# Optimization experiments

Measured on AMD Instinct MI355X. Metric: run time of the kernel, lower is better.

## Reference

```python
import jax, jax.numpy as jnp
import numpy as np

D = 64          # embed_dim
NH = 4          # nhead
DH = D // NH    # head dim
FF = 2048       # TransformerEncoderLayer default dim_feedforward
V = 1_000_000   # vocab (num items)
MAX_LEN = 50
INSERT_LEN = 10
EPS = 1e-5
N_LAYERS = 2


def setup_inputs() -> dict:
    key = jax.random.key(0)
    ks = jax.random.split(key, 8)
    s = 0.02
    return {
        "ht": jax.random.normal(ks[0], (D,), dtype=jnp.float32),
        "item_emb": jax.random.normal(ks[1], (V, D), dtype=jnp.float32) * s,
        "pos_emb": jax.random.normal(ks[2], (MAX_LEN, D), dtype=jnp.float32) * s,
        "in_proj_w": jax.random.normal(ks[3], (N_LAYERS, 3 * D, D), dtype=jnp.float32) * s,
        "in_proj_b": jnp.zeros((N_LAYERS, 3 * D), jnp.float32),
        "out_w": jax.random.normal(ks[4], (N_LAYERS, D, D), dtype=jnp.float32) * s,
        "out_b": jnp.zeros((N_LAYERS, D), jnp.float32),
        "ln1_w": jnp.ones((N_LAYERS, D), jnp.float32),
        "ln1_b": jnp.zeros((N_LAYERS, D), jnp.float32),
        "ln2_w": jnp.ones((N_LAYERS, D), jnp.float32),
        "ln2_b": jnp.zeros((N_LAYERS, D), jnp.float32),
        "ffn1_w": jax.random.normal(ks[5], (N_LAYERS, FF, D), dtype=jnp.float32) * s,
        "ffn1_b": jnp.zeros((N_LAYERS, FF), jnp.float32),
        "ffn2_w": jax.random.normal(ks[6], (N_LAYERS, D, FF), dtype=jnp.float32) * s,
        "ffn2_b": jnp.zeros((N_LAYERS, D), jnp.float32),
    }


def _ln(x, w, b):
    m = jnp.mean(x, axis=-1, keepdims=True)
    v = jnp.mean(jnp.square(x - m), axis=-1, keepdims=True)
    return (x - m) * jax.lax.rsqrt(v + EPS) * w + b


def _encoder_layer(x, ipw, ipb, ow, ob, l1w, l1b, l2w, l2b, f1w, f1b, f2w, f2b):
    # x: [S, D]; post-norm TransformerEncoderLayer (PyTorch defaults, eval mode)
    S = x.shape[0]
    qkv = x @ ipw.T + ipb                      # [S, 3D]
    q, k, v = jnp.split(qkv, 3, axis=-1)
    q = q.reshape(S, NH, DH)
    k = k.reshape(S, NH, DH)
    v = v.reshape(S, NH, DH)
    scores = jnp.einsum('shd,thd->hst', q, k) / jnp.sqrt(jnp.float32(DH))
    attn = jax.nn.softmax(scores, axis=-1)
    o = jnp.einsum('hst,thd->shd', attn, v).reshape(S, D)
    o = o @ ow.T + ob
    x = _ln(x + o, l1w, l1b)
    ff = jax.nn.relu(x @ f1w.T + f1b) @ f2w.T + f2b
    return _ln(x + ff, l2w, l2b)


def reference(ht, item_emb, pos_emb, in_proj_w, in_proj_b, out_w, out_b,
              ln1_w, ln1_b, ln2_w, ln2_b, ffn1_w, ffn1_b, ffn2_w, ffn2_b):
    gen = []         # generated item indices (traced int scalars)
    logits_all = []
    for _ in range(INSERT_LEN):
        if gen:
            gen_embed = item_emb[jnp.stack(gen)]             # [t, D]
            stack = jnp.concatenate([ht[None, :], gen_embed], axis=0)
        else:
            stack = ht[None, :]
        S = stack.shape[0]
        x = stack + pos_emb[:S]
        for l in range(N_LAYERS):
            x = _encoder_layer(x, in_proj_w[l], in_proj_b[l], out_w[l], out_b[l],
                               ln1_w[l], ln1_b[l], ln2_w[l], ln2_b[l],
                               ffn1_w[l], ffn1_b[l], ffn2_w[l], ffn2_b[l])
        logits = x[-1] @ item_emb.T                           # [V]
        gen.append(jnp.argmax(logits))
        logits_all.append(logits)
    return jnp.stack(logits_all), jnp.stack(gen)
```

## Files before the change

### kernel.cpp

```cpp
#include <hip/hip_runtime.h>

typedef unsigned long long u64;
typedef unsigned int u32;

#define V_ 1000000
#define STEPS_ 10
#define EPS_ 1e-5f
#define MARGIN_ 0.06f
#define FP8_SCALE 2048.0f
#define FP8_INV (1.0f / 2048.0f)
#define NCH 8192
#define CH 123
#define NBLK 64

__device__ __forceinline__ u64 pack_best(float v, int idx) {
    u32 u = __float_as_uint(v);
    u = (u & 0x80000000u) ? ~u : (u | 0x80000000u);
    return ((u64)u << 32) | (u64)(~(u32)idx);
}
__device__ __forceinline__ int unpack_idx(u64 p) { return (int)(~(u32)p); }
__device__ __forceinline__ float unpack_val(u64 p) {
    u32 hi = (u32)(p >> 32);
    return __uint_as_float((hi & 0x80000000u) ? (hi ^ 0x80000000u) : ~hi);
}
__device__ __forceinline__ u64 shfl_xor_u64(u64 v, int m) {
    u32 lo = (u32)v, hi = (u32)(v >> 32);
    lo = (u32)__shfl_xor((int)lo, m);
    hi = (u32)__shfl_xor((int)hi, m);
    return ((u64)hi << 32) | lo;
}

#define FP8_DOT16(u, q, p) do { \
    auto a0 = __builtin_amdgcn_cvt_pk_f32_fp8((u).x, false); \
    auto a1 = __builtin_amdgcn_cvt_pk_f32_fp8((u).x, true);  \
    auto b0 = __builtin_amdgcn_cvt_pk_f32_fp8((u).y, false); \
    auto b1 = __builtin_amdgcn_cvt_pk_f32_fp8((u).y, true);  \
    auto c0 = __builtin_amdgcn_cvt_pk_f32_fp8((u).z, false); \
    auto c1 = __builtin_amdgcn_cvt_pk_f32_fp8((u).z, true);  \
    auto d0 = __builtin_amdgcn_cvt_pk_f32_fp8((u).w, false); \
    auto d1 = __builtin_amdgcn_cvt_pk_f32_fp8((u).w, true);  \
    p = q[0]*a0[0] + q[1]*a0[1] + q[2]*a1[0] + q[3]*a1[1] \
      + q[4]*b0[0] + q[5]*b0[1] + q[6]*b1[0] + q[7]*b1[1] \
      + q[8]*c0[0] + q[9]*c0[1] + q[10]*c1[0] + q[11]*c1[1] \
      + q[12]*d0[0] + q[13]*d0[1] + q[14]*d1[0] + q[15]*d1[1]; \
} while (0)

__device__ __forceinline__ void grid_bar(u32* ctr, u32 expect) {
    __syncthreads();
    if (threadIdx.x == 0) {
        __hip_atomic_fetch_add(ctr, 1u, __ATOMIC_RELEASE, __HIP_MEMORY_SCOPE_AGENT);
        while (__hip_atomic_load(ctr, __ATOMIC_RELAXED, __HIP_MEMORY_SCOPE_AGENT) < expect)
            __builtin_amdgcn_s_sleep(4);
        __builtin_amdgcn_fence(__ATOMIC_ACQUIRE, "agent");
    }
    __syncthreads();
}

__device__ int resolve_argmax(const u64* __restrict__ cand,
                              const u32* __restrict__ emb8,
                              const float* __restrict__ item_emb,
                              const float* __restrict__ y_last,
                              const float* __restrict__ lnw,
                              const float* __restrict__ lnb,
                              float* s_xl, int* s_list, int* s_qg, u64* s_wm,
                              int* s_cnt, int* s_qcnt, u64* s_best)
{
    const int tid = threadIdx.x;
    if (tid < 64) {
        float v = y_last[tid];
        float m = v;
        #pragma unroll
        for (int o = 1; o < 64; o <<= 1) m += __shfl_xor(m, o);
        m *= (1.f / 64.f);
        float df = v - m;
        float var = df * df;
        #pragma unroll
        for (int o = 1; o < 64; o <<= 1) var += __shfl_xor(var, o);
        var *= (1.f / 64.f);
        s_xl[tid] = df * (1.f / sqrtf(var + EPS_)) * lnw[tid] + lnb[tid];
    }
    if (tid == 0) { *s_cnt = 0; *s_qcnt = 0; *s_best = 0ull; }
    __syncthreads();

    u64 m = 0ull;
    for (int i = tid; i < NCH; i += 256) { u64 c = cand[i]; if (c > m) m = c; }
    #pragma unroll
    for (int o = 1; o < 64; o <<= 1) { u64 x = shfl_xor_u64(m, o); if (x > m) m = x; }
    if ((tid & 63) == 0) s_wm[tid >> 6] = m;
    __syncthreads();
    if (tid == 0) {
        u64 b = s_wm[0];
        for (int i = 1; i < 4; i++) if (s_wm[i] > b) b = s_wm[i];
        s_wm[0] = b;
    }
    __syncthreads();
    const float thr = unpack_val(s_wm[0]) - MARGIN_;

    for (int i = tid; i < NCH; i += 256) {
        if (unpack_val(cand[i]) >= thr) {
            int p = atomicAdd(s_qcnt, 1);
            if (p < 64) s_qg[p] = i;
        }
    }
    __syncthreads();
    int nq = *s_qcnt; if (nq > 64) nq = 64;

    {
        const int l4 = tid & 3, rl = tid >> 2;
        float q[16];
        #pragma unroll
        for (int i = 0; i < 16; i++) q[i] = s_xl[l4 * 16 + i] * FP8_INV;
        for (int ci = 0; ci < nq; ci++) {
            const int r0 = s_qg[ci] * CH;
            #pragma unroll
            for (int half = 0; half < 2; half++) {
                int loc = half * 64 + rl;
                int row = r0 + loc;
                if (loc < CH && row < V_) {
                    uint4 u = ((const uint4*)emb8)[(size_t)row * 4 + l4];
                    float p;
                    FP8_DOT16(u, q, p);
                    p += __shfl_xor(p, 1);
                    p += __shfl_xor(p, 2);
                    if (l4 == 0 && p >= thr - 1e-3f) {
                        int pp = atomicAdd(s_cnt, 1);
                        if (pp < 128) s_list[pp] = row;
                    }
                }
            }
        }
    }
    __syncthreads();
    int n = *s_cnt; if (n > 128) n = 128;

    const int wid = tid >> 6, lane = tid & 63;
    for (int c = wid; c < n; c += 4) {
        int row = s_list[c];
        float p = s_xl[lane] * item_emb[(size_t)row * 64 + lane];
        #pragma unroll
        for (int o = 1; o < 64; o <<= 1) p += __shfl_xor(p, o);
        if (lane == 0) atomicMax(s_best, pack_best(p, row));
    }
    __syncthreads();
    return unpack_idx(*s_best);
}

__global__ __launch_bounds__(256) void step_kernel(
    const float* __restrict__ ht, const float* __restrict__ item_emb,
    const float* __restrict__ pos_emb,
    const float* __restrict__ ipw, const float* __restrict__ ipb,
    const float* __restrict__ ow, const float* __restrict__ ob,
    const float* __restrict__ l1w, const float* __restrict__ l1b,
    const float* __restrict__ l2w, const float* __restrict__ l2b,
    const float* __restrict__ f1w, const float* __restrict__ f1b,
    const float* __restrict__ f2w, const float* __restrict__ f2b,
    const u64* __restrict__ cand, const u32* __restrict__ emb8,
    float* __restrict__ y_last,
    int* __restrict__ gen_idx, float* __restrict__ gen_out,
    float* __restrict__ y0, float* __restrict__ hbuf, float* __restrict__ hbuf2,
    u32* __restrict__ bar, int t)
{
    const int S = t + 1;
    const int tid = threadIdx.x, bid = blockIdx.x;
    __shared__ __align__(16) float x[640], qkv[1920], o_[640], y2[640], xps[640];
    __shared__ __align__(16) float xpl[64];
    __shared__ float att[400], rm[10], rr[10], sw[4][10], xl[64], ol[64], y2l[64];
    __shared__ int list[128], qg[64], cnt, qcnt;
    __shared__ u64 wm[4], best;

    const float* ipw1 = ipw + 192 * 64;  const float* ipb1 = ipb + 192;
    const float* ow1  = ow + 64 * 64;    const float* ob1  = ob + 64;
    const float* l1w1 = l1w + 64;        const float* l1b1 = l1b + 64;
    const float* l2w1 = l2w + 64;        const float* l2b1 = l2b + 64;
    const float* f1w1 = f1w + 2048 * 64; const float* f1b1 = f1b + 2048;
    const float* f2w1 = f2w + (size_t)64 * 2048; const float* f2b1 = f2b + 64;

    int newidx = -1;
    if (t > 0) {
        newidx = resolve_argmax(cand, emb8, item_emb, y_last, l2w1, l2b1,
                                xl, list, qg, wm, &cnt, &qcnt, &best);
        if (bid == 0 && tid == 0) { gen_idx[t - 1] = newidx; gen_out[t - 1] = (float)newidx; }
    }
    __syncthreads();

    for (int i = tid; i < S * 64; i += 256) {
        int s = i >> 6, d = i & 63;
        float base;
        if (s == 0) base = ht[d];
        else {
            int gi = (s == t) ? newidx : gen_idx[s - 1];
            base = item_emb[(size_t)gi * 64 + d];
        }
        x[i] = base + pos_emb[i];
    }
    __syncthreads();

    for (int i = tid; i < S * 192; i += 256) {
        int s = i / 192, j2 = i % 192;
        float acc = ipb[j2];
        const float4* wr = (const float4*)(ipw + j2 * 64);
        const float4* xr = (const float4*)(x + s * 64);
        #pragma unroll
        for (int k = 0; k < 16; k++) {
            float4 w4 = wr[k], xv = xr[k];
            acc += w4.x * xv.x + w4.y * xv.y + w4.z * xv.z + w4.w * xv.w;
        }
        qkv[i] = acc;
    }
    __syncthreads();

    for (int i = tid; i < 4 * S * S; i += 256) {
        int h = i / (S * S), r = i % (S * S);
        int si = r / S, ti = r % S;
        const float* qr = qkv + si * 192 + h * 16;
        const float* kr = qkv + ti * 192 + 64 + h * 16;
        float acc = 0.f;
        #pragma unroll
        for (int k = 0; k < 16; k++) acc += qr[k] * kr[k];
        att[(h * S + si) * S + ti] = acc * 0.25f;
    }
    __syncthreads();
    for (int i = tid; i < 4 * S; i += 256) {
        float* row = att + i * S;
        float mx = row[0];
        for (int j2 = 1; j2 < S; j2++) mx = fmaxf(mx, row[j2]);
        float sm = 0.f;
        for (int j2 = 0; j2 < S; j2++) { float e = expf(row[j2] - mx); row[j2] = e; sm += e; }
        float inv = 1.f / sm;
        for (int j2 = 0; j2 < S; j2++) row[j2] *= inv;
    }
    __syncthreads();
    for (int i = tid; i < S * 64; i += 256) {
        int si = i >> 6, d = i & 63, h = d >> 4, dh = d & 15;
        const float* ar = att + (h * S + si) * S;
        float acc = 0.f;
        for (int ti = 0; ti < S; ti++) acc += ar[ti] * qkv[ti * 192 + 128 + h * 16 + dh];
        o_[i] = acc;
    }
    __syncthreads();
    for (int i = tid; i < S * 64; i += 256) {
        int s = i >> 6, d = i & 63;
        float acc = ob[d] + x[i];
        const float4* wr = (const float4*)(ow + d * 64);
        const float4* orow = (const float4*)(o_ + s * 64);
        #pragma unroll
        for (int k = 0; k < 16; k++) {
            float4 w4 = wr[k], ov = orow[k];
            acc += w4.x * ov.x + w4.y * ov.y + w4.z * ov.z + w4.w * ov.w;
        }
        y2[i] = acc;
    }
    __syncthreads();
    if (tid < S) {
        const float* yr = y2 + tid * 64;
        float m = 0.f;
        for (int k = 0; k < 64; k++) m += yr[k];
        m *= (1.f / 64.f);
        float v = 0.f;
        for (int k = 0; k < 64; k++) { float df = yr[k] - m; v += df * df; }
        rm[tid] = m;
        rr[tid] = 1.f / sqrtf(v * (1.f / 64.f) + EPS_);
    }
    __syncthreads();
    for (int i = tid; i < S * 64; i += 256) {
        int s = i >> 6, d = i & 63;
        xps[i] = (y2[i] - rm[s]) * rr[s] * l1w[d] + l1b[d];
    }
    __syncthreads();

    const int jl = tid >> 3, kp = tid & 7;
    const int j = bid * 32 + jl;
    {
        const float4* wr = (const float4*)(f1w + (size_t)j * 64);
        float4 wa = wr[kp * 2], wb = wr[kp * 2 + 1];
        float b1 = f1b[j];
        for (int s = 0; s < S; s++) {
            const float4* xr = (const float4*)(xps + s * 64);
            float4 xa = xr[kp * 2], xb = xr[kp * 2 + 1];
            float p = wa.x * xa.x + wa.y * xa.y + wa.z * xa.z + wa.w * xa.w
                    + wb.x * xb.x + wb.y * xb.y + wb.z * xb.z + wb.w * xb.w;
            p += __shfl_xor(p, 1);
            p += __shfl_xor(p, 2);
            p += __shfl_xor(p, 4);
            if (kp == 0) hbuf[s * 2048 + j] = fmaxf(p + b1, 0.f);
        }
    }
    grid_bar(bar + t * 4 + 0, NBLK);

    {
        const int d = bid;
        const float4* w4 = (const float4*)(f2w + (size_t)d * 2048 + tid * 8);
        float4 w0 = w4[0], w1 = w4[1];
        for (int s = 0; s < S; s++) {
            const float4* h4 = (const float4*)(hbuf + s * 2048 + tid * 8);
            float4 h0 = h4[0], h1 = h4[1];
            float p = w0.x * h0.x + w0.y * h0.y + w0.z * h0.z + w0.w * h0.w
                    + w1.x * h1.x + w1.y * h1.y + w1.z * h1.z + w1.w * h1.w;
            #pragma unroll
            for (int o = 1; o < 64; o <<= 1) p += __shfl_xor(p, o);
            if ((tid & 63) == 0) sw[tid >> 6][s] = p;
        }
        __syncthreads();
        if (tid < S)
            y0[tid * 64 + d] = sw[0][tid] + sw[1][tid] + sw[2][tid] + sw[3][tid]
                             + f2b[d] + xps[tid * 64 + d];
    }
    grid_bar(bar + t * 4 + 1, NBLK);

    for (int i = tid; i < S * 64; i += 256) y2[i] = y0[i];
    __syncthreads();
    if (tid < S) {
        const float* yr = y2 + tid * 64;
        float m = 0.f;
        for (int k = 0; k < 64; k++) m += yr[k];
        m *= (1.f / 64.f);
        float v = 0.f;
        for (int k = 0; k < 64; k++) { float df = yr[k] - m; v += df * df; }
        rm[tid] = m;
        rr[tid] = 1.f / sqrtf(v * (1.f / 64.f) + EPS_);
    }
    __syncthreads();
    for (int i = tid; i < S * 64; i += 256) {
        int s = i >> 6, d = i & 63;
        x[i] = (y2[i] - rm[s]) * rr[s] * l2w[d] + l2b[d];
    }
    __syncthreads();

    for (int i = tid; i < S * 192; i += 256) {
        int s = i / 192, j2 = i % 192;
        float acc = ipb1[j2];
        const float4* wr = (const float4*)(ipw1 + j2 * 64);
        const float4* xr = (const float4*)(x + s * 64);
        #pragma unroll
        for (int k = 0; k < 16; k++) {
            float4 w4 = wr[k], xv = xr[k];
            acc += w4.x * xv.x + w4.y * xv.y + w4.z * xv.z + w4.w * xv.w;
        }
        qkv[i] = acc;
    }
    __syncthreads();

    for (int i = tid; i < 4 * S; i += 256) {
        int h = i / S, ti = i % S;
        const float* qr = qkv + (S - 1) * 192 + h * 16;
        const float* kr = qkv + ti * 192 + 64 + h * 16;
        float acc = 0.f;
        #pragma unroll
        for (int k = 0; k < 16; k++) acc += qr[k] * kr[k];
        att[h * S + ti] = acc * 0.25f;
    }
    __syncthreads();
    if (tid < 4) {
        float* row = att + tid * S;
        float mx = row[0];
        for (int j2 = 1; j2 < S; j2++) mx = fmaxf(mx, row[j2]);
        float sm = 0.f;
        for (int j2 = 0; j2 < S; j2++) { float e = expf(row[j2] - mx); row[j2] = e; sm += e; }
        float inv = 1.f / sm;
        for (int j2 = 0; j2 < S; j2++) row[j2] *= inv;
    }
    __syncthreads();
    if (tid < 64) {
        int h = tid >> 4, dh = tid & 15;
        const float* ar = att + h * S;
        float acc = 0.f;
        for (int ti = 0; ti < S; ti++) acc += ar[ti] * qkv[ti * 192 + 128 + h * 16 + dh];
        ol[tid] = acc;
    }
    __syncthreads();
    if (tid < 64) {
        float acc = ob1[tid] + x[(S - 1) * 64 + tid];
        const float* wr = ow1 + tid * 64;
        for (int k = 0; k < 64; k++) acc += ol[k] * wr[k];
        y2l[tid] = acc;
    }
    __syncthreads();
    if (tid < 64) {
        float v = y2l[tid];
        float m = v;
        #pragma unroll
        for (int o = 1; o < 64; o <<= 1) m += __shfl_xor(m, o);
        m *= (1.f / 64.f);
        float df = v - m;
        float var = df * df;
        #pragma unroll
        for (int o = 1; o < 64; o <<= 1) var += __shfl_xor(var, o);
        float r = 1.f / sqrtf(var * (1.f / 64.f) + EPS_);
        xpl[tid] = df * r * l1w1[tid] + l1b1[tid];
    }
    __syncthreads();

    {
        const float4* wr = (const float4*)(f1w1 + (size_t)j * 64);
        float4 wa = wr[kp * 2], wb = wr[kp * 2 + 1];
        const float4* xr = (const float4*)xpl;
        float4 xa = xr[kp * 2], xb = xr[kp * 2 + 1];
        float p = wa.x * xa.x + wa.y * xa.y + wa.z * xa.z + wa.w * xa.w
                + wb.x * xb.x + wb.y * xb.y + wb.z * xb.z + wb.w * xb.w;
        p += __shfl_xor(p, 1);
        p += __shfl_xor(p, 2);
        p += __shfl_xor(p, 4);
        if (kp == 0) hbuf2[j] = fmaxf(p + f1b1[j], 0.f);
    }
    grid_bar(bar + t * 4 + 2, NBLK);

    {
        const int d = bid;
        const float4* w4 = (const float4*)(f2w1 + (size_t)d * 2048 + tid * 8);
        const float4* h4 = (const float4*)(hbuf2 + tid * 8);
        float4 w0 = w4[0], w1 = w4[1], h0 = h4[0], h1 = h4[1];
        float p = w0.x * h0.x + w0.y * h0.y + w0.z * h0.z + w0.w * h0.w
                + w1.x * h1.x + w1.y * h1.y + w1.z * h1.z + w1.w * h1.w;
        #pragma unroll
        for (int o = 1; o < 64; o <<= 1) p += __shfl_xor(p, o);
        if ((tid & 63) == 0) sw[tid >> 6][0] = p;
        __syncthreads();
        if (tid == 0) y_last[d] = sw[0][0] + sw[1][0] + sw[2][0] + sw[3][0] + f2b1[d] + xpl[d];
    }
}

__global__ __launch_bounds__(256) void scan0_kernel(
    const float* __restrict__ item_emb, const float* __restrict__ y_last,
    const float* __restrict__ lnw, const float* __restrict__ lnb,
    u64* __restrict__ cand, float* __restrict__ xl_all, u32* __restrict__ emb8)
{
    const int tid = threadIdx.x;
    __shared__ float xl[64];
    if (tid < 64) {
        float v = y_last[tid];
        float m = v;
        #pragma unroll
        for (int o = 1; o < 64; o <<= 1) m += __shfl_xor(m, o);
        m *= (1.f / 64.f);
        float df = v - m;
        float var = df * df;
        #pragma unroll
        for (int o = 1; o < 64; o <<= 1) var += __shfl_xor(var, o);
        float r = 1.f / sqrtf(var * (1.f / 64.f) + EPS_);
        float v_ = df * r * lnw[tid] + lnb[tid];
        xl[tid] = v_;
        if (blockIdx.x == 0) xl_all[tid] = v_;
    }
    __syncthreads();

    const int lane = tid & 63, wid = tid >> 6;
    const int g = blockIdx.x * 4 + wid;
    const int l16 = lane & 15, rl = lane >> 4;
    float4 q = ((const float4*)xl)[l16];
    const int r0 = g * CH;
    u64 lb = 0ull;
    for (int it = 0; it < 31; it++) {
        int loc = it * 4 + rl;
        int row = r0 + loc;
        if (loc < CH && row < V_) {
            float4 e = ((const float4*)(item_emb + (size_t)row * 64))[l16];
            u32 pk8 = (u32)__builtin_amdgcn_cvt_pk_fp8_f32(e.x * FP8_SCALE, e.y * FP8_SCALE, 0, false);
            pk8 = (u32)__builtin_amdgcn_cvt_pk_fp8_f32(e.z * FP8_SCALE, e.w * FP8_SCALE, (int)pk8, true);
            emb8[(size_t)row * 16 + l16] = pk8;
            float p = q.x * e.x + q.y * e.y + q.z * e.z + q.w * e.w;
            p += __shfl_xor(p, 1);
            p += __shfl_xor(p, 2);
            p += __shfl_xor(p, 4);
            p += __shfl_xor(p, 8);
            if (l16 == 0) { u64 pk = pack_best(p, row); if (pk > lb) lb = pk; }
        }
    }
    #pragma unroll
    for (int o = 1; o < 64; o <<= 1) { u64 xv = shfl_xor_u64(lb, o); if (xv > lb) lb = xv; }
    if (lane == 0) cand[g] = lb;
}

__global__ __launch_bounds__(256) void scan_fp8_kernel(
    const u32* __restrict__ emb8, const float* __restrict__ y_last,
    const float* __restrict__ lnw, const float* __restrict__ lnb,
    u64* __restrict__ cand, float* __restrict__ xl_all, int t)
{
    const int tid = threadIdx.x;
    __shared__ float xls[64];
    if (tid < 64) {
        float v = y_last[tid];
        float m = v;
        #pragma unroll
        for (int o = 1; o < 64; o <<= 1) m += __shfl_xor(m, o);
        m *= (1.f / 64.f);
        float df = v - m;
        float var = df * df;
        #pragma unroll
        for (int o = 1; o < 64; o <<= 1) var += __shfl_xor(var, o);
        float r = 1.f / sqrtf(var * (1.f / 64.f) + EPS_);
        float v_ = df * r * lnw[tid] + lnb[tid];
        if (blockIdx.x == 0) xl_all[t * 64 + tid] = v_;
        xls[tid] = v_ * FP8_INV;
    }
    __syncthreads();

    const int lane = tid & 63, wid = tid >> 6;
    const int g = blockIdx.x * 4 + wid;
    const int l4 = lane & 3, rl = lane >> 2;
    float q[16];
    #pragma unroll
    for (int i = 0; i < 16; i++) q[i] = xls[l4 * 16 + i];
    const int r0 = g * CH;
    u64 lb = 0ull;
    for (int it = 0; it < 8; it++) {
        int loc = it * 16 + rl;
        int row = r0 + loc;
        if (loc < CH && row < V_) {
            uint4 u = ((const uint4*)emb8)[(size_t)row * 4 + l4];
            float p;
            FP8_DOT16(u, q, p);
            p += __shfl_xor(p, 1);
            p += __shfl_xor(p, 2);
            if (l4 == 0) { u64 pk = pack_best(p, row); if (pk > lb) lb = pk; }
        }
    }
    #pragma unroll
    for (int o = 1; o < 64; o <<= 1) { u64 xv = shfl_xor_u64(lb, o); if (xv > lb) lb = xv; }
    if (lane == 0) cand[g] = lb;
}

__global__ __launch_bounds__(256) void finalize_kernel(
    const u64* __restrict__ cand, const u32* __restrict__ emb8,
    const float* __restrict__ item_emb, const float* __restrict__ y_last,
    const float* __restrict__ lnw, const float* __restrict__ lnb,
    float* __restrict__ gen_out)
{
    __shared__ float xl[64];
    __shared__ int list[128], qg[64], cnt, qcnt;
    __shared__ u64 wm[4], best;
    int r = resolve_argmax(cand, emb8, item_emb, y_last, lnw, lnb,
                           xl, list, qg, wm, &cnt, &qcnt, &best);
    if (threadIdx.x == 0) gen_out[STEPS_ - 1] = (float)r;
}

__global__ __launch_bounds__(256) void logits_all_kernel(
    const float* __restrict__ item_emb, const float* __restrict__ xl_all,
    float* __restrict__ out)
{
    const int tid = threadIdx.x;
    const int lane = tid & 63, wv = tid >> 6;
    const int l4 = lane & 3, qd = lane >> 2;

    float4 qv[10][4];
    #pragma unroll
    for (int p = 0; p < 10; p++) {
        #pragma unroll
        for (int c = 0; c < 4; c++)
            qv[p][c] = *(const float4*)(xl_all + p * 64 + l4 * 16 + c * 4);
    }

    const int row_in_blk = wv * 16 + qd;
    for (int tile = blockIdx.x; tile < V_ / 64; tile += gridDim.x) {
        const int row = tile * 64 + row_in_blk;
        const float4* er = (const float4*)(item_emb + (size_t)row * 64 + l4 * 16);
        float4 e0 = er[0], e1 = er[1], e2 = er[2], e3 = er[3];
        float acc[10];
        #pragma unroll
        for (int p = 0; p < 10; p++) {
            float s = qv[p][0].x*e0.x + qv[p][0].y*e0.y + qv[p][0].z*e0.z + qv[p][0].w*e0.w
                    + qv[p][1].x*e1.x + qv[p][1].y*e1.y + qv[p][1].z*e1.z + qv[p][1].w*e1.w
                    + qv[p][2].x*e2.x + qv[p][2].y*e2.y + qv[p][2].z*e2.z + qv[p][2].w*e2.w
                    + qv[p][3].x*e3.x + qv[p][3].y*e3.y + qv[p][3].z*e3.z + qv[p][3].w*e3.w;
            s += __shfl_xor(s, 1);
            s += __shfl_xor(s, 2);
            acc[p] = s;
        }
        if (l4 == 0) {
            #pragma unroll
            for (int p = 0; p < 10; p++)
                out[(size_t)p * V_ + row] = acc[p];
        }
    }
}

extern "C" void kernel_launch(void* const* d_in, const int* in_sizes, int n_in,
                              void* d_out, int out_size, void* d_ws, size_t ws_size,
                              hipStream_t stream) {
    const float* ht       = (const float*)d_in[0];
    const float* item_emb = (const float*)d_in[1];
    const float* pos_emb  = (const float*)d_in[2];
    const float* ipw      = (const float*)d_in[3];
    const float* ipb      = (const float*)d_in[4];
    const float* ow       = (const float*)d_in[5];
    const float* ob       = (const float*)d_in[6];
    const float* l1w      = (const float*)d_in[7];
    const float* l1b      = (const float*)d_in[8];
    const float* l2w      = (const float*)d_in[9];
    const float* l2b      = (const float*)d_in[10];
    const float* f1w      = (const float*)d_in[11];
    const float* f1b      = (const float*)d_in[12];
    const float* f2w      = (const float*)d_in[13];
    const float* f2b      = (const float*)d_in[14];

    float* out = (float*)d_out;
    char* ws = (char*)d_ws;
    int*   gen_idx = (int*)ws;
    float* y_last  = (float*)(ws + 64);
    float* y0      = (float*)(ws + 512);
    float* hbuf2   = (float*)(ws + 3072);
    float* xl_all  = (float*)(ws + 11264);
    u32*   bar     = (u32*)(ws + 14336);
    float* hbuf    = (float*)(ws + 16384);
    u64*   cand    = (u64*)(ws + 131072);
    u32*   emb8    = (u32*)(ws + 262144);
    float* gen_out = out + (size_t)STEPS_ * V_;

    hipMemsetAsync(bar, 0, 256, stream);

    for (int t = 0; t < STEPS_; t++) {
        step_kernel<<<NBLK, 256, 0, stream>>>(
            ht, item_emb, pos_emb, ipw, ipb, ow, ob, l1w, l1b, l2w, l2b,
            f1w, f1b, f2w, f2b, cand, emb8, y_last, gen_idx, gen_out,
            y0, hbuf, hbuf2, bar, t);
        if (t == 0)
            scan0_kernel<<<2048, 256, 0, stream>>>(
                item_emb, y_last, l2w + 64, l2b + 64, cand, xl_all, emb8);
        else
            scan_fp8_kernel<<<2048, 256, 0, stream>>>(
                emb8, y_last, l2w + 64, l2b + 64, cand, xl_all, t);
    }
    finalize_kernel<<<1, 256, 0, stream>>>(
        cand, emb8, item_emb, y_last, l2w + 64, l2b + 64, gen_out);
    logits_all_kernel<<<2048, 256, 0, stream>>>(item_emb, xl_all, out);
}
```

Measured before the change: 1.177 ms.

## Fuse all decode steps, scans and logits into one persistent megakernel

Replaces the per-step sequence of step, scan, finalize and logits kernels with a single persistent 1024-block kernel. Grid-wide sync uses hierarchical tree barriers, and a 64-block sub-barrier covers the transformer part. The argmax resolve is split across the 64 step blocks and combined with a global atomicMax. The aim is to remove about 22 kernel launches and their serialization gaps. In exchange it relies on all blocks being co-resident for the spin barriers, and adds a poll-count bailout that could silently break correctness if that assumption fails.

Measured after the change: 2.151 ms. 82.8% more time.

```diff
diff --git a/kernel.cpp b/kernel.cpp
--- a/kernel.cpp
+++ b/kernel.cpp
@@ -11,7 +11,9 @@
 #define FP8_INV (1.0f / 2048.0f)
 #define NCH 8192
 #define CH 123
-#define NBLK 64
+#define GRID_ 1024
+#define NSTEP_BLK 64
+#define BAIL_ (1u << 21)
 
 __device__ __forceinline__ u64 pack_best(float v, int idx) {
     u32 u = __float_as_uint(v);
@@ -45,107 +47,39 @@
       + q[12]*d0[0] + q[13]*d0[1] + q[14]*d1[0] + q[15]*d1[1]; \
 } while (0)
 
-__device__ __forceinline__ void grid_bar(u32* ctr, u32 expect) {
+__device__ __forceinline__ void sub_bar(u32* ctr, u32 expect) {
     __syncthreads();
     if (threadIdx.x == 0) {
-        __hip_atomic_fetch_add(ctr, 1u, __ATOMIC_RELEASE, __HIP_MEMORY_SCOPE_AGENT);
-        while (__hip_atomic_load(ctr, __ATOMIC_RELAXED, __HIP_MEMORY_SCOPE_AGENT) < expect)
-            __builtin_amdgcn_s_sleep(4);
+        __hip_atomic_fetch_add(ctr, 1u, __ATOMIC_ACQ_REL, __HIP_MEMORY_SCOPE_AGENT);
+        u32 polls = 0;
+        while (__hip_atomic_load(ctr, __ATOMIC_RELAXED, __HIP_MEMORY_SCOPE_AGENT) < expect) {
+            __builtin_amdgcn_s_sleep(8);
+            if (++polls > BAIL_) break;
+        }
         __builtin_amdgcn_fence(__ATOMIC_ACQUIRE, "agent");
     }
     __syncthreads();
 }
 
-__device__ int resolve_argmax(const u64* __restrict__ cand,
-                              const u32* __restrict__ emb8,
-                              const float* __restrict__ item_emb,
-                              const float* __restrict__ y_last,
-                              const float* __restrict__ lnw,
-                              const float* __restrict__ lnb,
-                              float* s_xl, int* s_list, int* s_qg, u64* s_wm,
-                              int* s_cnt, int* s_qcnt, u64* s_best)
-{
-    const int tid = threadIdx.x;
-    if (tid < 64) {
-        float v = y_last[tid];
-        float m = v;
-        #pragma unroll
-        for (int o = 1; o < 64; o <<= 1) m += __shfl_xor(m, o);
-        m *= (1.f / 64.f);
-        float df = v - m;
-        float var = df * df;
-        #pragma unroll
-        for (int o = 1; o < 64; o <<= 1) var += __shfl_xor(var, o);
-        var *= (1.f / 64.f);
-        s_xl[tid] = df * (1.f / sqrtf(var + EPS_)) * lnw[tid] + lnb[tid];
-    }
-    if (tid == 0) { *s_cnt = 0; *s_qcnt = 0; *s_best = 0ull; }
+__device__ __forceinline__ void tree_bar(char* barbase, int inst, int bid) {
     __syncthreads();
-
-    u64 m = 0ull;
-    for (int i = tid; i < NCH; i += 256) { u64 c = cand[i]; if (c > m) m = c; }
-    #pragma unroll
-    for (int o = 1; o < 64; o <<= 1) { u64 x = shfl_xor_u64(m, o); if (x > m) m = x; }
-    if ((tid & 63) == 0) s_wm[tid >> 6] = m;
-    __syncthreads();
-    if (tid == 0) {
-        u64 b = s_wm[0];
-        for (int i = 1; i < 4; i++) if (s_wm[i] > b) b = s_wm[i];
-        s_wm[0] = b;
+    if (threadIdx.x == 0) {
+        u32* leaf = (u32*)(barbase + (size_t)inst * 4096 + (size_t)(bid >> 4) * 64);
+        u32* root = (u32*)(barbase + 81920 + (size_t)inst * 64);
+        u32 old = __hip_atomic_fetch_add(leaf, 1u, __ATOMIC_ACQ_REL, __HIP_MEMORY_SCOPE_AGENT);
+        if (old == 15u)
+            __hip_atomic_fetch_add(root, 1u, __ATOMIC_ACQ_REL, __HIP_MEMORY_SCOPE_AGENT);
+        u32 polls = 0;
+        while (__hip_atomic_load(root, __ATOMIC_RELAXED, __HIP_MEMORY_SCOPE_AGENT) < 64u) {
+            __builtin_amdgcn_s_sleep(16);
+            if (++polls > BAIL_) break;
+        }
+        __builtin_amdgcn_fence(__ATOMIC_ACQUIRE, "agent");
     }
     __syncthreads();
-    const float thr = unpack_val(s_wm[0]) - MARGIN_;
-
-    for (int i = tid; i < NCH; i += 256) {
-        if (unpack_val(cand[i]) >= thr) {
-            int p = atomicAdd(s_qcnt, 1);
-            if (p < 64) s_qg[p] = i;
-        }
-    }
-    __syncthreads();
-    int nq = *s_qcnt; if (nq > 64) nq = 64;
-
-    {
-        const int l4 = tid & 3, rl = tid >> 2;
-        float q[16];
-        #pragma unroll
-        for (int i = 0; i < 16; i++) q[i] = s_xl[l4 * 16 + i] * FP8_INV;
-        for (int ci = 0; ci < nq; ci++) {
-            const int r0 = s_qg[ci] * CH;
-            #pragma unroll
-            for (int half = 0; half < 2; half++) {
-                int loc = half * 64 + rl;
-                int row = r0 + loc;
-                if (loc < CH && row < V_) {
-                    uint4 u = ((const uint4*)emb8)[(size_t)row * 4 + l4];
-                    float p;
-                    FP8_DOT16(u, q, p);
-                    p += __shfl_xor(p, 1);
-                    p += __shfl_xor(p, 2);
-                    if (l4 == 0 && p >= thr - 1e-3f) {
-                        int pp = atomicAdd(s_cnt, 1);
-                        if (pp < 128) s_list[pp] = row;
-                    }
-                }
-            }
-        }
-    }
-    __syncthreads();
-    int n = *s_cnt; if (n > 128) n = 128;
-
-    const int wid = tid >> 6, lane = tid & 63;
-    for (int c = wid; c < n; c += 4) {
-        int row = s_list[c];
-        float p = s_xl[lane] * item_emb[(size_t)row * 64 + lane];
-        #pragma unroll
-        for (int o = 1; o < 64; o <<= 1) p += __shfl_xor(p, o);
-        if (lane == 0) atomicMax(s_best, pack_best(p, row));
-    }
-    __syncthreads();
-    return unpack_idx(*s_best);
 }
 
-__global__ __launch_bounds__(256) void step_kernel(
+__global__ __launch_bounds__(256, 4) void mega_kernel(
     const float* __restrict__ ht, const float* __restrict__ item_emb,
     const float* __restrict__ pos_emb,
     const float* __restrict__ ipw, const float* __restrict__ ipb,
@@ -154,19 +88,21 @@
     const float* __restrict__ l2w, const float* __restrict__ l2b,
     const float* __restrict__ f1w, const float* __restrict__ f1b,
     const float* __restrict__ f2w, const float* __restrict__ f2b,
-    const u64* __restrict__ cand, const u32* __restrict__ emb8,
-    float* __restrict__ y_last,
-    int* __restrict__ gen_idx, float* __restrict__ gen_out,
+    char* __restrict__ bar,
+    u64* __restrict__ cand, u32* __restrict__ emb8,
+    float* __restrict__ y_last, int* __restrict__ gen_idx,
     float* __restrict__ y0, float* __restrict__ hbuf, float* __restrict__ hbuf2,
-    u32* __restrict__ bar, int t)
+    float* __restrict__ xl_all,
+    float* __restrict__ out, float* __restrict__ gen_out)
 {
-    const int S = t + 1;
     const int tid = threadIdx.x, bid = blockIdx.x;
+    const int lane = tid & 63, wv = tid >> 6;
+
     __shared__ __align__(16) float x[640], qkv[1920], o_[640], y2[640], xps[640];
     __shared__ __align__(16) float xpl[64];
-    __shared__ float att[400], rm[10], rr[10], sw[4][10], xl[64], ol[64], y2l[64];
-    __shared__ int list[128], qg[64], cnt, qcnt;
-    __shared__ u64 wm[4], best;
+    __shared__ float att[400], rm[10], rr[10], sw[4][10], xl[64], ol[64], y2l[64], xls[64];
+    __shared__ int list[256], qg[128], cnt, qcnt;
+    __shared__ u64 wm[4], sbest;
 
     const float* ipw1 = ipw + 192 * 64;  const float* ipb1 = ipb + 192;
     const float* ow1  = ow + 64 * 64;    const float* ob1  = ob + 64;
@@ -174,401 +110,512 @@
     const float* l2w1 = l2w + 64;        const float* l2b1 = l2b + 64;
     const float* f1w1 = f1w + 2048 * 64; const float* f1b1 = f1b + 2048;
     const float* f2w1 = f2w + (size_t)64 * 2048; const float* f2b1 = f2b + 64;
-
-    int newidx = -1;
-    if (t > 0) {
-        newidx = resolve_argmax(cand, emb8, item_emb, y_last, l2w1, l2b1,
-                                xl, list, qg, wm, &cnt, &qcnt, &best);
-        if (bid == 0 && tid == 0) { gen_idx[t - 1] = newidx; gen_out[t - 1] = (float)newidx; }
+    u64* g_best = (u64*)(bar + 90112);
+
+    for (int t = 0; t < STEPS_; ++t) {
+        const int S = t + 1;
+
+        if (bid < NSTEP_BLK) {
+            int newidx = -1;
+            if (t > 0) {
+                if (tid < 64) {
+                    float v = y_last[tid];
+                    float m = v;
+                    #pragma unroll
+                    for (int o = 1; o < 64; o <<= 1) m += __shfl_xor(m, o);
+                    m *= (1.f / 64.f);
+                    float df = v - m;
+                    float var = df * df;
+                    #pragma unroll
+                    for (int o = 1; o < 64; o <<= 1) var += __shfl_xor(var, o);
+                    var *= (1.f / 64.f);
+                    xl[tid] = df * (1.f / sqrtf(var + EPS_)) * l2w1[tid] + l2b1[tid];
+                }
+                if (tid == 0) { cnt = 0; qcnt = 0; sbest = 0ull; }
+                __syncthreads();
+
+                u64 m = 0ull;
+                for (int i = tid; i < NCH; i += 256) { u64 c = cand[i]; if (c > m) m = c; }
+                #pragma unroll
+                for (int o = 1; o < 64; o <<= 1) { u64 xv = shfl_xor_u64(m, o); if (xv > m) m = xv; }
+                if (lane == 0) wm[wv] = m;
+                __syncthreads();
+                if (tid == 0) {
+                    u64 b = wm[0];
+                    for (int i = 1; i < 4; i++) if (wm[i] > b) b = wm[i];
+                    wm[0] = b;
+                }
+                __syncthreads();
+                const float thr = unpack_val(wm[0]) - MARGIN_;
+
+                for (int i = tid; i < NCH; i += 256) {
+                    if ((i & 63) == bid && unpack_val(cand[i]) >= thr) {
+                        int p = atomicAdd(&qcnt, 1);
+                        if (p < 128) qg[p] = i;
+                    }
+                }
+                __syncthreads();
+                int nq = qcnt; if (nq > 128) nq = 128;
+
+                {
+                    const int l4 = tid & 3, rl = tid >> 2;
+                    float q[16];
+                    #pragma unroll
+                    for (int i = 0; i < 16; i++) q[i] = xl[l4 * 16 + i] * FP8_INV;
+                    for (int ci = 0; ci < nq; ci++) {
+                        const int r0 = qg[ci] * CH;
+                        #pragma unroll
+                        for (int half = 0; half < 2; half++) {
+                            int loc = half * 64 + rl;
+                            int row = r0 + loc;
+                            if (loc < CH && row < V_) {
+                                uint4 u = ((const uint4*)emb8)[(size_t)row * 4 + l4];
+                                float p;
+                                FP8_DOT16(u, q, p);
+                                p += __shfl_xor(p, 1);
+                                p += __shfl_xor(p, 2);
+                                if (l4 == 0 && p >= thr - 1e-3f) {
+                                    int pp = atomicAdd(&cnt, 1);
+                                    if (pp < 256) list[pp] = row;
+                                }
+                            }
+                        }
+                    }
+                }
+                __syncthreads();
+                int n = cnt; if (n > 256) n = 256;
+
+                for (int c = wv; c < n; c += 4) {
+                    int row = list[c];
+                    float p = xl[lane] * item_emb[(size_t)row * 64 + lane];
+                    #pragma unroll
+                    for (int o = 1; o < 64; o <<= 1) p += __shfl_xor(p, o);
+                    if (lane == 0) atomicMax(&sbest, pack_best(p, row));
+                }
+                __syncthreads();
+                if (tid == 0 && sbest) atomicMax(&g_best[t], sbest);
+                sub_bar((u32*)(bar + 83968 + (size_t)(t * 4 + 0) * 64), NSTEP_BLK);
+                u64 gb = __hip_atomic_load(&g_best[t], __ATOMIC_RELAXED, __HIP_MEMORY_SCOPE_AGENT);
+                newidx = unpack_idx(gb);
+                if (bid == 0 && tid == 0) {
+                    gen_idx[t - 1] = newidx;
+                    gen_out[t - 1] = (float)newidx;
+                }
+            }
+            __syncthreads();
+
+            for (int i = tid; i < S * 64; i += 256) {
+                int s = i >> 6, d = i & 63;
+                float base;
+                if (s == 0) base = ht[d];
+                else base = item_emb[(size_t)((s == t) ? newidx : gen_idx[s - 1]) * 64 + d];
+                x[i] = base + pos_emb[i];
+            }
+            __syncthreads();
+
+            for (int i = tid; i < S * 192; i += 256) {
+                int s = i / 192, j2 = i % 192;
+                float acc = ipb[j2];
+                const float4* wr = (const float4*)(ipw + j2 * 64);
+                const float4* xr = (const float4*)(x + s * 64);
+                #pragma unroll
+                for (int k = 0; k < 16; k++) {
+                    float4 w4 = wr[k], xv = xr[k];
+                    acc += w4.x * xv.x + w4.y * xv.y + w4.z * xv.z + w4.w * xv.w;
+                }
+                qkv[i] = acc;
+            }
+            __syncthreads();
+
+            for (int i = tid; i < 4 * S * S; i += 256) {
+                int h = i / (S * S), r = i % (S * S);
+                int si = r / S, ti = r % S;
+                const float* qr = qkv + si * 192 + h * 16;
+                const float* kr = qkv + ti * 192 + 64 + h * 16;
+                float acc = 0.f;
+                #pragma unroll
+                for (int k = 0; k < 16; k++) acc += qr[k] * kr[k];
+                att[(h * S + si) * S + ti] = acc * 0.25f;
+            }
+            __syncthreads();
+            if (tid < 4 * S) {
+                float* row = att + tid * S;
+                float mx = row[0];
+                for (int j2 = 1; j2 < S; j2++) mx = fmaxf(mx, row[j2]);
+                float sm = 0.f;
+                for (int j2 = 0; j2 < S; j2++) { float e = expf(row[j2] - mx); row[j2] = e; sm += e; }
+                float inv = 1.f / sm;
+                for (int j2 = 0; j2 < S; j2++) row[j2] *= inv;
+            }
+            __syncthreads();
+            for (int i = tid; i < S * 64; i += 256) {
+                int si = i >> 6, d = i & 63, h = d >> 4, dh = d & 15;
+                const float* ar = att + (h * S + si) * S;
+                float acc = 0.f;
+                for (int ti = 0; ti < S; ti++) acc += ar[ti] * qkv[ti * 192 + 128 + h * 16 + dh];
+                o_[i] = acc;
+            }
+            __syncthreads();
+            for (int i = tid; i < S * 64; i += 256) {
+                int s = i >> 6, d = i & 63;
+                float acc = ob[d] + x[i];
+                const float4* wr = (const float4*)(ow + d * 64);
+                const float4* orow = (const float4*)(o_ + s * 64);
+                #pragma unroll
+                for (int k = 0; k < 16; k++) {
+                    float4 w4 = wr[k], ov = orow[k];
+                    acc += w4.x * ov.x + w4.y * ov.y + w4.z * ov.z + w4.w * ov.w;
+                }
+                y2[i] = acc;
+            }
+            __syncthreads();
+            if (tid < S) {
+                const float* yr = y2 + tid * 64;
+                float m = 0.f;
+                for (int k = 0; k < 64; k++) m += yr[k];
+                m *= (1.f / 64.f);
+                float v = 0.f;
+                for (int k = 0; k < 64; k++) { float df = yr[k] - m; v += df * df; }
+                rm[tid] = m;
+                rr[tid] = 1.f / sqrtf(v * (1.f / 64.f) + EPS_);
+            }
+            __syncthreads();
+            for (int i = tid; i < S * 64; i += 256) {
+                int s = i >> 6, d = i & 63;
+                xps[i] = (y2[i] - rm[s]) * rr[s] * l1w[d] + l1b[d];
+            }
+            __syncthreads();
+
+            const int jl = tid >> 3, kp = tid & 7;
+            const int j = bid * 32 + jl;
+            {
+                const float4* wr = (const float4*)(f1w + (size_t)j * 64);
+                float4 wa = wr[kp * 2], wb = wr[kp * 2 + 1];
+                float b1 = f1b[j];
+                for (int s = 0; s < S; s++) {
+                    const float4* xr = (const float4*)(xps + s * 64);
+                    float4 xa = xr[kp * 2], xb = xr[kp * 2 + 1];
+                    float p = wa.x * xa.x + wa.y * xa.y + wa.z * xa.z + wa.w * xa.w
+                            + wb.x * xb.x + wb.y * xb.y + wb.z * xb.z + wb.w * xb.w;
+                    p += __shfl_xor(p, 1);
+                    p += __shfl_xor(p, 2);
+                    p += __shfl_xor(p, 4);
+                    if (kp == 0) hbuf[s * 2048 + j] = fmaxf(p + b1, 0.f);
+                }
+            }
+            sub_bar((u32*)(bar + 83968 + (size_t)(t * 4 + 1) * 64), NSTEP_BLK);
+
+            {
+                const int d = bid;
+                const float4* w4 = (const float4*)(f2w + (size_t)d * 2048 + tid * 8);
+                float4 w0 = w4[0], w1 = w4[1];
+                for (int s = 0; s < S; s++) {
+                    const float4* h4 = (const float4*)(hbuf + s * 2048 + tid * 8);
+                    float4 h0 = h4[0], h1 = h4[1];
+                    float p = w0.x * h0.x + w0.y * h0.y + w0.z * h0.z + w0.w * h0.w
+                            + w1.x * h1.x + w1.y * h1.y + w1.z * h1.z + w1.w * h1.w;
+                    #pragma unroll
+                    for (int o = 1; o < 64; o <<= 1) p += __shfl_xor(p, o);
+                    if (lane == 0) sw[wv][s] = p;
+                }
+                __syncthreads();
+                if (tid < S)
+                    y0[tid * 64 + d] = sw[0][tid] + sw[1][tid] + sw[2][tid] + sw[3][tid]
+                                     + f2b[d] + xps[tid * 64 + d];
+            }
+            sub_bar((u32*)(bar + 83968 + (size_t)(t * 4 + 2) * 64), NSTEP_BLK);
+
+            for (int i = tid; i < S * 64; i += 256) y2[i] = y0[i];
+            __syncthreads();
+            if (tid < S) {
+                const float* yr = y2 + tid * 64;
+                float m = 0.f;
+                for (int k = 0; k < 64; k++) m += yr[k];
+                m *= (1.f / 64.f);
+                float v = 0.f;
+                for (int k = 0; k < 64; k++) { float df = yr[k] - m; v += df * df; }
+                rm[tid] = m;
+                rr[tid] = 1.f / sqrtf(v * (1.f / 64.f) + EPS_);
+            }
+            __syncthreads();
+            for (int i = tid; i < S * 64; i += 256) {
+                int s = i >> 6, d = i & 63;
+                x[i] = (y2[i] - rm[s]) * rr[s] * l2w[d] + l2b[d];
+            }
+            __syncthreads();
+
+            for (int i = tid; i < S * 192; i += 256) {
+                int s = i / 192, j2 = i % 192;
+                float acc = ipb1[j2];
+                const float4* wr = (const float4*)(ipw1 + j2 * 64);
+                const float4* xr = (const float4*)(x + s * 64);
+                #pragma unroll
+                for (int k = 0; k < 16; k++) {
+                    float4 w4 = wr[k], xv = xr[k];
+                    acc += w4.x * xv.x + w4.y * xv.y + w4.z * xv.z + w4.w * xv.w;
+                }
+                qkv[i] = acc;
+            }
+            __syncthreads();
+
+            if (tid < 4 * S) {
+                int h = tid / S, ti = tid % S;
+                const float* qr = qkv + (S - 1) * 192 + h * 16;
+                const float* kr = qkv + ti * 192 + 64 + h * 16;
+                float acc = 0.f;
+                #pragma unroll
+                for (int k = 0; k < 16; k++) acc += qr[k] * kr[k];
+                att[h * S + ti] = acc * 0.25f;
+            }
+            __syncthreads();
+            if (tid < 4) {
+                float* row = att + tid * S;
+                float mx = row[0];
+                for (int j2 = 1; j2 < S; j2++) mx = fmaxf(mx, row[j2]);
+                float sm = 0.f;
+                for (int j2 = 0; j2 < S; j2++) { float e = expf(row[j2] - mx); row[j2] = e; sm += e; }
+                float inv = 1.f / sm;
+                for (int j2 = 0; j2 < S; j2++) row[j2] *= inv;
+            }
+            __syncthreads();
+            if (tid < 64) {
+                int h = tid >> 4, dh = tid & 15;
+                const float* ar = att + h * S;
+                float acc = 0.f;
+                for (int ti = 0; ti < S; ti++) acc += ar[ti] * qkv[ti * 192 + 128 + h * 16 + dh];
+                ol[tid] = acc;
+            }
+            __syncthreads();
+            if (tid < 64) {
+                float acc = ob1[tid] + x[(S - 1) * 64 + tid];
+                const float* wr = ow1 + tid * 64;
+                for (int k = 0; k < 64; k++) acc += ol[k] * wr[k];
+                y2l[tid] = acc;
+            }
+            __syncthreads();
+            if (tid < 64) {
+                float v = y2l[tid];
+                float m = v;
+                #pragma unroll
+                for (int o = 1; o < 64; o <<= 1) m += __shfl_xor(m, o);
+                m *= (1.f / 64.f);
+                float df = v - m;
+                float var = df * df;
+                #pragma unroll
+                for (int o = 1; o < 64; o <<= 1) var += __shfl_xor(var, o);
+                float r = 1.f / sqrtf(var * (1.f / 64.f) + EPS_);
+                xpl[tid] = df * r * l1w1[tid] + l1b1[tid];
+            }
+            __syncthreads();
+
+            {
+                const float4* wr = (const float4*)(f1w1 + (size_t)j * 64);
+                float4 wa = wr[kp * 2], wb = wr[kp * 2 + 1];
+                const float4* xr = (const float4*)xpl;
+                float4 xa = xr[kp * 2], xb = xr[kp * 2 + 1];
+                float p = wa.x * xa.x + wa.y * xa.y + wa.z * xa.z + wa.w * xa.w
+                        + wb.x * xb.x + wb.y * xb.y + wb.z * xb.z + wb.w * xb.w;
+                p += __shfl_xor(p, 1);
+                p += __shfl_xor(p, 2);
+                p += __shfl_xor(p, 4);
+                if (kp == 0) hbuf2[j] = fmaxf(p + f1b1[j], 0.f);
+            }
+            sub_bar((u32*)(bar + 83968 + (size_t)(t * 4 + 3) * 64), NSTEP_BLK);
+
+            {
+                const int d = bid;
+                const float4* w4 = (const float4*)(f2w1 + (size_t)d * 2048 + tid * 8);
+                const float4* h4 = (const float4*)(hbuf2 + tid * 8);
+                float4 w0 = w4[0], w1 = w4[1], h0 = h4[0], h1 = h4[1];
+                float p = w0.x * h0.x + w0.y * h0.y + w0.z * h0.z + w0.w * h0.w
+                        + w1.x * h1.x + w1.y * h1.y + w1.z * h1.z + w1.w * h1.w;
+                #pragma unroll
+                for (int o = 1; o < 64; o <<= 1) p += __shfl_xor(p, o);
+                if (lane == 0) sw[wv][0] = p;
+                __syncthreads();
+                if (tid == 0)
+                    y_last[d] = sw[0][0] + sw[1][0] + sw[2][0] + sw[3][0] + f2b1[d] + xpl[d];
+            }
+        }
+
+        tree_bar(bar, 2 * t, bid);
+
+        if (tid < 64) {
+            float v = y_last[tid];
+            float m = v;
+            #pragma unroll
+            for (int o = 1; o < 64; o <<= 1) m += __shfl_xor(m, o);
+            m *= (1.f / 64.f);
+            float df = v - m;
+            float var = df * df;
+            #pragma unroll
+            for (int o = 1; o < 64; o <<= 1) var += __shfl_xor(var, o);
+            float r = 1.f / sqrtf(var * (1.f / 64.f) + EPS_);
+            float v_ = df * r * l2w1[tid] + l2b1[tid];
+            xls[tid] = (t == 0) ? v_ : v_ * FP8_INV;
+            if (bid == 0) xl_all[t * 64 + tid] = v_;
+        }
+        __syncthreads();
+
+        const int wgid = bid * 4 + wv;
+        if (t == 0) {
+            const int l16 = lane & 15, rl = lane >> 4;
+            float4 q = ((const float4*)xls)[l16];
+            for (int g = wgid; g < NCH; g += GRID_ * 4) {
+                const int r0 = g * CH;
+                u64 lb = 0ull;
+                for (int it = 0; it < 31; it++) {
+                    int loc = it * 4 + rl;
+                    int row = r0 + loc;
+                    if (loc < CH && row < V_) {
+                        float4 e = ((const float4*)(item_emb + (size_t)row * 64))[l16];
+                        u32 pk8 = (u32)__builtin_amdgcn_cvt_pk_fp8_f32(e.x * FP8_SCALE, e.y * FP8_SCALE, 0, false);
+                        pk8 = (u32)__builtin_amdgcn_cvt_pk_fp8_f32(e.z * FP8_SCALE, e.w * FP8_SCALE, (int)pk8, true);
+                        emb8[(size_t)row * 16 + l16] = pk8;
+                        float p = q.x * e.x + q.y * e.y + q.z * e.z + q.w * e.w;
+                        p += __shfl_xor(p, 1);
+                        p += __shfl_xor(p, 2);
+                        p += __shfl_xor(p, 4);
+                        p += __shfl_xor(p, 8);
+                        if (l16 == 0) { u64 pk = pack_best(p, row); if (pk > lb) lb = pk; }
+                    }
+                }
+                #pragma unroll
+                for (int o = 1; o < 64; o <<= 1) { u64 xv = shfl_xor_u64(lb, o); if (xv > lb) lb = xv; }
+                if (lane == 0) cand[g] = lb;
+            }
+        } else {
+            const int l4 = lane & 3, rl = lane >> 2;
+            float q[16];
+            #pragma unroll
+            for (int i = 0; i < 16; i++) q[i] = xls[l4 * 16 + i];
+            for (int g = wgid; g < NCH; g += GRID_ * 4) {
+                const int r0 = g * CH;
+                u64 lb = 0ull;
+                for (int it = 0; it < 8; it++) {
+                    int loc = it * 16 + rl;
+                    int row = r0 + loc;
+                    if (loc < CH && row < V_) {
+                        uint4 u = ((const uint4*)emb8)[(size_t)row * 4 + l4];
+                        float p;
+                        FP8_DOT16(u, q, p);
+                        p += __shfl_xor(p, 1);
+                        p += __shfl_xor(p, 2);
+                        if (l4 == 0) { u64 pk = pack_best(p, row); if (pk > lb) lb = pk; }
+                    }
+                }
+                #pragma unroll
+                for (int o = 1; o < 64; o <<= 1) { u64 xv = shfl_xor_u64(lb, o); if (xv > lb) lb = xv; }
+                if (lane == 0) cand[g] = lb;
+            }
+        }
+
+        tree_bar(bar, 2 * t + 1, bid);
     }
+
+    if (bid < NSTEP_BLK) {
+        if (tid < 64) {
+            float v = y_last[tid];
+            float m = v;
+            #pragma unroll
+            for (int o = 1; o < 64; o <<= 1) m += __shfl_xor(m, o);
+            m *= (1.f / 64.f);
+            float df = v - m;
+            float var = df * df;
+            #pragma unroll
+            for (int o = 1; o < 64; o <<= 1) var += __shfl_xor(var, o);
+            var *= (1.f / 64.f);
+            xl[tid] = df * (1.f / sqrtf(var + EPS_)) * l2w1[tid] + l2b1[tid];
+        }
+        if (tid == 0) { cnt = 0; qcnt = 0; sbest = 0ull; }
+        __syncthreads();
+
+        u64 m = 0ull;
+        for (int i = tid; i < NCH; i += 256) { u64 c = cand[i]; if (c > m) m = c; }
+        #pragma unroll
+        for (int o = 1; o < 64; o <<= 1) { u64 xv = shfl_xor_u64(m, o); if (xv > m) m = xv; }
+        if (lane == 0) wm[wv] = m;
+        __syncthreads();
+        if (tid == 0) {
+            u64 b = wm[0];
+            for (int i = 1; i < 4; i++) if (wm[i] > b) b = wm[i];
+            wm[0] = b;
+        }
+        __syncthreads();
+        const float thr = unpack_val(wm[0]) - MARGIN_;
+
+        for (int i = tid; i < NCH; i += 256) {
+            if ((i & 63) == bid && unpack_val(cand[i]) >= thr) {
+                int p = atomicAdd(&qcnt, 1);
+                if (p < 128) qg[p] = i;
+            }
+        }
+        __syncthreads();
+        int nq = qcnt; if (nq > 128) nq = 128;
+        {
+            const int l4 = tid & 3, rl = tid >> 2;
+            float q[16];
+            #pragma unroll
+            for (int i = 0; i < 16; i++) q[i] = xl[l4 * 16 + i] * FP8_INV;
+            for (int ci = 0; ci < nq; ci++) {
+                const int r0 = qg[ci] * CH;
+                #pragma unroll
+                for (int half = 0; half < 2; half++) {
+                    int loc = half * 64 + rl;
+                    int row = r0 + loc;
+                    if (loc < CH && row < V_) {
+                        uint4 u = ((const uint4*)emb8)[(size_t)row * 4 + l4];
+                        float p;
+                        FP8_DOT16(u, q, p);
+                        p += __shfl_xor(p, 1);
+                        p += __shfl_xor(p, 2);
+                        if (l4 == 0 && p >= thr - 1e-3f) {
+                            int pp = atomicAdd(&cnt, 1);
+                            if (pp < 256) list[pp] = row;
+                        }
+                    }
+                }
+            }
+        }
+        __syncthreads();
+        int n = cnt; if (n > 256) n = 256;
+        for (int c = wv; c < n; c += 4) {
+            int row = list[c];
+            float p = xl[lane] * item_emb[(size_t)row * 64 + lane];
+            #pragma unroll
+            for (int o = 1; o < 64; o <<= 1) p += __shfl_xor(p, o);
+            if (lane == 0) atomicMax(&sbest, pack_best(p, row));
+        }
+        __syncthreads();
+        if (tid == 0 && sbest) atomicMax(&g_best[10], sbest);
+        sub_bar((u32*)(bar + 83968 + (size_t)40 * 64), NSTEP_BLK);
+        if (bid == 0 && tid == 0) {
+            u64 gb = __hip_atomic_load(&g_best[10], __ATOMIC_RELAXED, __HIP_MEMORY_SCOPE_AGENT);
+            gen_out[STEPS_ - 1] = (float)unpack_idx(gb);
+        }
+    }
+
+    for (int i = tid; i < 640; i += 256) x[i] = xl_all[i];
     __syncthreads();
-
-    for (int i = tid; i < S * 64; i += 256) {
-        int s = i >> 6, d = i & 63;
-        float base;
-        if (s == 0) base = ht[d];
-        else {
-            int gi = (s == t) ? newidx : gen_idx[s - 1];
-            base = item_emb[(size_t)gi * 64 + d];
-        }
-        x[i] = base + pos_emb[i];
-    }
-    __syncthreads();
-
-    for (int i = tid; i < S * 192; i += 256) {
-        int s = i / 192, j2 = i % 192;
-        float acc = ipb[j2];
-        const float4* wr = (const float4*)(ipw + j2 * 64);
-        const float4* xr = (const float4*)(x + s * 64);
-        #pragma unroll
-        for (int k = 0; k < 16; k++) {
-            float4 w4 = wr[k], xv = xr[k];
-            acc += w4.x * xv.x + w4.y * xv.y + w4.z * xv.z + w4.w * xv.w;
-        }
-        qkv[i] = acc;
-    }
-    __syncthreads();
-
-    for (int i = tid; i < 4 * S * S; i += 256) {
-        int h = i / (S * S), r = i % (S * S);
-        int si = r / S, ti = r % S;
-        const float* qr = qkv + si * 192 + h * 16;
-        const float* kr = qkv + ti * 192 + 64 + h * 16;
-        float acc = 0.f;
-        #pragma unroll
-        for (int k = 0; k < 16; k++) acc += qr[k] * kr[k];
-        att[(h * S + si) * S + ti] = acc * 0.25f;
-    }
-    __syncthreads();
-    for (int i = tid; i < 4 * S; i += 256) {
-        float* row = att + i * S;
-        float mx = row[0];
-        for (int j2 = 1; j2 < S; j2++) mx = fmaxf(mx, row[j2]);
-        float sm = 0.f;
-        for (int j2 = 0; j2 < S; j2++) { float e = expf(row[j2] - mx); row[j2] = e; sm += e; }
-        float inv = 1.f / sm;
-        for (int j2 = 0; j2 < S; j2++) row[j2] *= inv;
-    }
-    __syncthreads();
-    for (int i = tid; i < S * 64; i += 256) {
-        int si = i >> 6, d = i & 63, h = d >> 4, dh = d & 15;
-        const float* ar = att + (h * S + si) * S;
-        float acc = 0.f;
-        for (int ti = 0; ti < S; ti++) acc += ar[ti] * qkv[ti * 192 + 128 + h * 16 + dh];
-        o_[i] = acc;
-    }
-    __syncthreads();
-    for (int i = tid; i < S * 64; i += 256) {
-        int s = i >> 6, d = i & 63;
-        float acc = ob[d] + x[i];
-        const float4* wr = (const float4*)(ow + d * 64);
-        const float4* orow = (const float4*)(o_ + s * 64);
-        #pragma unroll
-        for (int k = 0; k < 16; k++) {
-            float4 w4 = wr[k], ov = orow[k];
-            acc += w4.x * ov.x + w4.y * ov.y + w4.z * ov.z + w4.w * ov.w;
-        }
-        y2[i] = acc;
-    }
-    __syncthreads();
-    if (tid < S) {
-        const float* yr = y2 + tid * 64;
-        float m = 0.f;
-        for (int k = 0; k < 64; k++) m += yr[k];
-        m *= (1.f / 64.f);
-        float v = 0.f;
-        for (int k = 0; k < 64; k++) { float df = yr[k] - m; v += df * df; }
-        rm[tid] = m;
-        rr[tid] = 1.f / sqrtf(v * (1.f / 64.f) + EPS_);
-    }
-    __syncthreads();
-    for (int i = tid; i < S * 64; i += 256) {
-        int s = i >> 6, d = i & 63;
-        xps[i] = (y2[i] - rm[s]) * rr[s] * l1w[d] + l1b[d];
-    }
-    __syncthreads();
-
-    const int jl = tid >> 3, kp = tid & 7;
-    const int j = bid * 32 + jl;
     {
-        const float4* wr = (const float4*)(f1w + (size_t)j * 64);
-        float4 wa = wr[kp * 2], wb = wr[kp * 2 + 1];
-        float b1 = f1b[j];
-        for (int s = 0; s < S; s++) {
-            const float4* xr = (const float4*)(xps + s * 64);
-            float4 xa = xr[kp * 2], xb = xr[kp * 2 + 1];
-            float p = wa.x * xa.x + wa.y * xa.y + wa.z * xa.z + wa.w * xa.w
-                    + wb.x * xb.x + wb.y * xb.y + wb.z * xb.z + wb.w * xb.w;
-            p += __shfl_xor(p, 1);
-            p += __shfl_xor(p, 2);
-            p += __shfl_xor(p, 4);
-            if (kp == 0) hbuf[s * 2048 + j] = fmaxf(p + b1, 0.f);
-        }
-    }
-    grid_bar(bar + t * 4 + 0, NBLK);
-
-    {
-        const int d = bid;
-        const float4* w4 = (const float4*)(f2w + (size_t)d * 2048 + tid * 8);
-        float4 w0 = w4[0], w1 = w4[1];
-        for (int s = 0; s < S; s++) {
-            const float4* h4 = (const float4*)(hbuf + s * 2048 + tid * 8);
-            float4 h0 = h4[0], h1 = h4[1];
-            float p = w0.x * h0.x + w0.y * h0.y + w0.z * h0.z + w0.w * h0.w
-                    + w1.x * h1.x + w1.y * h1.y + w1.z * h1.z + w1.w * h1.w;
-            #pragma unroll
-            for (int o = 1; o < 64; o <<= 1) p += __shfl_xor(p, o);
-            if ((tid & 63) == 0) sw[tid >> 6][s] = p;
-        }
-        __syncthreads();
-        if (tid < S)
-            y0[tid * 64 + d] = sw[0][tid] + sw[1][tid] + sw[2][tid] + sw[3][tid]
-                             + f2b[d] + xps[tid * 64 + d];
-    }
-    grid_bar(bar + t * 4 + 1, NBLK);
-
-    for (int i = tid; i < S * 64; i += 256) y2[i] = y0[i];
-    __syncthreads();
-    if (tid < S) {
-        const float* yr = y2 + tid * 64;
-        float m = 0.f;
-        for (int k = 0; k < 64; k++) m += yr[k];
-        m *= (1.f / 64.f);
-        float v = 0.f;
-        for (int k = 0; k < 64; k++) { float df = yr[k] - m; v += df * df; }
-        rm[tid] = m;
-        rr[tid] = 1.f / sqrtf(v * (1.f / 64.f) + EPS_);
-    }
-    __syncthreads();
-    for (int i = tid; i < S * 64; i += 256) {
-        int s = i >> 6, d = i & 63;
-        x[i] = (y2[i] - rm[s]) * rr[s] * l2w[d] + l2b[d];
-    }
-    __syncthreads();
-
-    for (int i = tid; i < S * 192; i += 256) {
-        int s = i / 192, j2 = i % 192;
-        float acc = ipb1[j2];
-        const float4* wr = (const float4*)(ipw1 + j2 * 64);
-        const float4* xr = (const float4*)(x + s * 64);
-        #pragma unroll
-        for (int k = 0; k < 16; k++) {
-            float4 w4 = wr[k], xv = xr[k];
-            acc += w4.x * xv.x + w4.y * xv.y + w4.z * xv.z + w4.w * xv.w;
-        }
-        qkv[i] = acc;
-    }
-    __syncthreads();
-
-    for (int i = tid; i < 4 * S; i += 256) {
-        int h = i / S, ti = i % S;
-        const float* qr = qkv + (S - 1) * 192 + h * 16;
-        const float* kr = qkv + ti * 192 + 64 + h * 16;
-        float acc = 0.f;
-        #pragma unroll
-        for (int k = 0; k < 16; k++) acc += qr[k] * kr[k];
-        att[h * S + ti] = acc * 0.25f;
-    }
-    __syncthreads();
-    if (tid < 4) {
-        float* row = att + tid * S;
-        float mx = row[0];
-        for (int j2 = 1; j2 < S; j2++) mx = fmaxf(mx, row[j2]);
-        float sm = 0.f;
-        for (int j2 = 0; j2 < S; j2++) { float e = expf(row[j2] - mx); row[j2] = e; sm += e; }
-        float inv = 1.f / sm;
-        for (int j2 = 0; j2 < S; j2++) row[j2] *= inv;
-    }
-    __syncthreads();
-    if (tid < 64) {
-        int h = tid >> 4, dh = tid & 15;
-        const float* ar = att + h * S;
-        float acc = 0.f;
-        for (int ti = 0; ti < S; ti++) acc += ar[ti] * qkv[ti * 192 + 128 + h * 16 + dh];
-        ol[tid] = acc;
-    }
-    __syncthreads();
-    if (tid < 64) {
-        float acc = ob1[tid] + x[(S - 1) * 64 + tid];
-        const float* wr = ow1 + tid * 64;
-        for (int k = 0; k < 64; k++) acc += ol[k] * wr[k];
-        y2l[tid] = acc;
-    }
-    __syncthreads();
-    if (tid < 64) {
-        float v = y2l[tid];
-        float m = v;
-        #pragma unroll
-        for (int o = 1; o < 64; o <<= 1) m += __shfl_xor(m, o);
-        m *= (1.f / 64.f);
-        float df = v - m;
-        float var = df * df;
-        #pragma unroll
-        for (int o = 1; o < 64; o <<= 1) var += __shfl_xor(var, o);
-        float r = 1.f / sqrtf(var * (1.f / 64.f) + EPS_);
-        xpl[tid] = df * r * l1w1[tid] + l1b1[tid];
-    }
-    __syncthreads();
-
-    {
-        const float4* wr = (const float4*)(f1w1 + (size_t)j * 64);
-        float4 wa = wr[kp * 2], wb = wr[kp * 2 + 1];
-        const float4* xr = (const float4*)xpl;
-        float4 xa = xr[kp * 2], xb = xr[kp * 2 + 1];
-        float p = wa.x * xa.x + wa.y * xa.y + wa.z * xa.z + wa.w * xa.w
-                + wb.x * xb.x + wb.y * xb.y + wb.z * xb.z + wb.w * xb.w;
-        p += __shfl_xor(p, 1);
-        p += __shfl_xor(p, 2);
-        p += __shfl_xor(p, 4);
-        if (kp == 0) hbuf2[j] = fmaxf(p + f1b1[j], 0.f);
-    }
-    grid_bar(bar + t * 4 + 2, NBLK);
-
-    {
-        const int d = bid;
-        const float4* w4 = (const float4*)(f2w1 + (size_t)d * 2048 + tid * 8);
-        const float4* h4 = (const float4*)(hbuf2 + tid * 8);
-        float4 w0 = w4[0], w1 = w4[1], h0 = h4[0], h1 = h4[1];
-        float p = w0.x * h0.x + w0.y * h0.y + w0.z * h0.z + w0.w * h0.w
-                + w1.x * h1.x + w1.y * h1.y + w1.z * h1.z + w1.w * h1.w;
-        #pragma unroll
-        for (int o = 1; o < 64; o <<= 1) p += __shfl_xor(p, o);
-        if ((tid & 63) == 0) sw[tid >> 6][0] = p;
-        __syncthreads();
-        if (tid == 0) y_last[d] = sw[0][0] + sw[1][0] + sw[2][0] + sw[3][0] + f2b1[d] + xpl[d];
-    }
-}
-
-__global__ __launch_bounds__(256) void scan0_kernel(
-    const float* __restrict__ item_emb, const float* __restrict__ y_last,
-    const float* __restrict__ lnw, const float* __restrict__ lnb,
-    u64* __restrict__ cand, float* __restrict__ xl_all, u32* __restrict__ emb8)
-{
-    const int tid = threadIdx.x;
-    __shared__ float xl[64];
-    if (tid < 64) {
-        float v = y_last[tid];
-        float m = v;
-        #pragma unroll
-        for (int o = 1; o < 64; o <<= 1) m += __shfl_xor(m, o);
-        m *= (1.f / 64.f);
-        float df = v - m;
-        float var = df * df;
-        #pragma unroll
-        for (int o = 1; o < 64; o <<= 1) var += __shfl_xor(var, o);
-        float r = 1.f / sqrtf(var * (1.f / 64.f) + EPS_);
-        float v_ = df * r * lnw[tid] + lnb[tid];
-        xl[tid] = v_;
-        if (blockIdx.x == 0) xl_all[tid] = v_;
-    }
-    __syncthreads();
-
-    const int lane = tid & 63, wid = tid >> 6;
-    const int g = blockIdx.x * 4 + wid;
-    const int l16 = lane & 15, rl = lane >> 4;
-    float4 q = ((const float4*)xl)[l16];
-    const int r0 = g * CH;
-    u64 lb = 0ull;
-    for (int it = 0; it < 31; it++) {
-        int loc = it * 4 + rl;
-        int row = r0 + loc;
-        if (loc < CH && row < V_) {
-            float4 e = ((const float4*)(item_emb + (size_t)row * 64))[l16];
-            u32 pk8 = (u32)__builtin_amdgcn_cvt_pk_fp8_f32(e.x * FP8_SCALE, e.y * FP8_SCALE, 0, false);
-            pk8 = (u32)__builtin_amdgcn_cvt_pk_fp8_f32(e.z * FP8_SCALE, e.w * FP8_SCALE, (int)pk8, true);
-            emb8[(size_t)row * 16 + l16] = pk8;
-            float p = q.x * e.x + q.y * e.y + q.z * e.z + q.w * e.w;
-            p += __shfl_xor(p, 1);
-            p += __shfl_xor(p, 2);
-            p += __shfl_xor(p, 4);
-            p += __shfl_xor(p, 8);
-            if (l16 == 0) { u64 pk = pack_best(p, row); if (pk > lb) lb = pk; }
-        }
-    }
-    #pragma unroll
-    for (int o = 1; o < 64; o <<= 1) { u64 xv = shfl_xor_u64(lb, o); if (xv > lb) lb = xv; }
-    if (lane == 0) cand[g] = lb;
-}
-
-__global__ __launch_bounds__(256) void scan_fp8_kernel(
-    const u32* __restrict__ emb8, const float* __restrict__ y_last,
-    const float* __restrict__ lnw, const float* __restrict__ lnb,
-    u64* __restrict__ cand, float* __restrict__ xl_all, int t)
-{
-    const int tid = threadIdx.x;
-    __shared__ float xls[64];
-    if (tid < 64) {
-        float v = y_last[tid];
-        float m = v;
-        #pragma unroll
-        for (int o = 1; o < 64; o <<= 1) m += __shfl_xor(m, o);
-        m *= (1.f / 64.f);
-        float df = v - m;
-        float var = df * df;
-        #pragma unroll
-        for (int o = 1; o < 64; o <<= 1) var += __shfl_xor(var, o);
-        float r = 1.f / sqrtf(var * (1.f / 64.f) + EPS_);
-        float v_ = df * r * lnw[tid] + lnb[tid];
-        if (blockIdx.x == 0) xl_all[t * 64 + tid] = v_;
-        xls[tid] = v_ * FP8_INV;
-    }
-    __syncthreads();
-
-    const int lane = tid & 63, wid = tid >> 6;
-    const int g = blockIdx.x * 4 + wid;
-    const int l4 = lane & 3, rl = lane >> 2;
-    float q[16];
-    #pragma unroll
-    for (int i = 0; i < 16; i++) q[i] = xls[l4 * 16 + i];
-    const int r0 = g * CH;
-    u64 lb = 0ull;
-    for (int it = 0; it < 8; it++) {
-        int loc = it * 16 + rl;
-        int row = r0 + loc;
-        if (loc < CH && row < V_) {
-            uint4 u = ((const uint4*)emb8)[(size_t)row * 4 + l4];
-            float p;
-            FP8_DOT16(u, q, p);
-            p += __shfl_xor(p, 1);
-            p += __shfl_xor(p, 2);
-            if (l4 == 0) { u64 pk = pack_best(p, row); if (pk > lb) lb = pk; }
-        }
-    }
-    #pragma unroll
-    for (int o = 1; o < 64; o <<= 1) { u64 xv = shfl_xor_u64(lb, o); if (xv > lb) lb = xv; }
-    if (lane == 0) cand[g] = lb;
-}
-
-__global__ __launch_bounds__(256) void finalize_kernel(
-    const u64* __restrict__ cand, const u32* __restrict__ emb8,
-    const float* __restrict__ item_emb, const float* __restrict__ y_last,
-    const float* __restrict__ lnw, const float* __restrict__ lnb,
-    float* __restrict__ gen_out)
-{
-    __shared__ float xl[64];
-    __shared__ int list[128], qg[64], cnt, qcnt;
-    __shared__ u64 wm[4], best;
-    int r = resolve_argmax(cand, emb8, item_emb, y_last, lnw, lnb,
-                           xl, list, qg, wm, &cnt, &qcnt, &best);
-    if (threadIdx.x == 0) gen_out[STEPS_ - 1] = (float)r;
-}
-
-__global__ __launch_bounds__(256) void logits_all_kernel(
-    const float* __restrict__ item_emb, const float* __restrict__ xl_all,
-    float* __restrict__ out)
-{
-    const int tid = threadIdx.x;
-    const int lane = tid & 63, wv = tid >> 6;
-    const int l4 = lane & 3, qd = lane >> 2;
-
-    float4 qv[10][4];
-    #pragma unroll
-    for (int p = 0; p < 10; p++) {
-        #pragma unroll
-        for (int c = 0; c < 4; c++)
-            qv[p][c] = *(const float4*)(xl_all + p * 64 + l4 * 16 + c * 4);
-    }
-
-    const int row_in_blk = wv * 16 + qd;
-    for (int tile = blockIdx.x; tile < V_ / 64; tile += gridDim.x) {
-        const int row = tile * 64 + row_in_blk;
-        const float4* er = (const float4*)(item_emb + (size_t)row * 64 + l4 * 16);
-        float4 e0 = er[0], e1 = er[1], e2 = er[2], e3 = er[3];
-        float acc[10];
-        #pragma unroll
-        for (int p = 0; p < 10; p++) {
-            float s = qv[p][0].x*e0.x + qv[p][0].y*e0.y + qv[p][0].z*e0.z + qv[p][0].w*e0.w
-                    + qv[p][1].x*e1.x + qv[p][1].y*e1.y + qv[p][1].z*e1.z + qv[p][1].w*e1.w
-                    + qv[p][2].x*e2.x + qv[p][2].y*e2.y + qv[p][2].z*e2.z + qv[p][2].w*e2.w
-                    + qv[p][3].x*e3.x + qv[p][3].y*e3.y + qv[p][3].z*e3.z + qv[p][3].w*e3.w;
-            s += __shfl_xor(s, 1);
-            s += __shfl_xor(s, 2);
-            acc[p] = s;
-        }
-        if (l4 == 0) {
-            #pragma unroll
-            for (int p = 0; p < 10; p++)
-                out[(size_t)p * V_ + row] = acc[p];
+        const int l4 = lane & 3, qd = lane >> 2;
+        const int row_in_blk = wv * 16 + qd;
+        for (int tile = bid; tile < V_ / 64; tile += GRID_) {
+            const int row = tile * 64 + row_in_blk;
+            const float4* er = (const float4*)(item_emb + (size_t)row * 64 + l4 * 16);
+            float4 e0 = er[0], e1 = er[1], e2 = er[2], e3 = er[3];
+            #pragma unroll
+            for (int p = 0; p < 10; p++) {
+                const float4* qr = (const float4*)(x + p * 64 + l4 * 16);
+                float4 q0 = qr[0], q1 = qr[1], q2 = qr[2], q3 = qr[3];
+                float s = q0.x*e0.x + q0.y*e0.y + q0.z*e0.z + q0.w*e0.w
+                        + q1.x*e1.x + q1.y*e1.y + q1.z*e1.z + q1.w*e1.w
+                        + q2.x*e2.x + q2.y*e2.y + q2.z*e2.z + q2.w*e2.w
+                        + q3.x*e3.x + q3.y*e3.y + q3.z*e3.z + q3.w*e3.w;
+                s += __shfl_xor(s, 1);
+                s += __shfl_xor(s, 2);
+                if (l4 == 0) out[(size_t)p * V_ + row] = s;
+            }
         }
     }
 }
@@ -596,30 +643,19 @@
     char* ws = (char*)d_ws;
     int*   gen_idx = (int*)ws;
     float* y_last  = (float*)(ws + 64);
-    float* y0      = (float*)(ws + 512);
-    float* hbuf2   = (float*)(ws + 3072);
-    float* xl_all  = (float*)(ws + 11264);
-    u32*   bar     = (u32*)(ws + 14336);
-    float* hbuf    = (float*)(ws + 16384);
+    float* y0      = (float*)(ws + 1024);
+    float* hbuf2   = (float*)(ws + 4096);
+    float* xl_all  = (float*)(ws + 12288);
+    char*  bar     = ws + 16384;
     u64*   cand    = (u64*)(ws + 131072);
-    u32*   emb8    = (u32*)(ws + 262144);
+    float* hbuf    = (float*)(ws + 196608);
+    u32*   emb8    = (u32*)(ws + 524288);
     float* gen_out = out + (size_t)STEPS_ * V_;
 
-    hipMemsetAsync(bar, 0, 256, stream);
-
-    for (int t = 0; t < STEPS_; t++) {
-        step_kernel<<<NBLK, 256, 0, stream>>>(
-            ht, item_emb, pos_emb, ipw, ipb, ow, ob, l1w, l1b, l2w, l2b,
-            f1w, f1b, f2w, f2b, cand, emb8, y_last, gen_idx, gen_out,
-            y0, hbuf, hbuf2, bar, t);
-        if (t == 0)
-            scan0_kernel<<<2048, 256, 0, stream>>>(
-                item_emb, y_last, l2w + 64, l2b + 64, cand, xl_all, emb8);
-        else
-            scan_fp8_kernel<<<2048, 256, 0, stream>>>(
-                emb8, y_last, l2w + 64, l2b + 64, cand, xl_all, t);
-    }
-    finalize_kernel<<<1, 256, 0, stream>>>(
-        cand, emb8, item_emb, y_last, l2w + 64, l2b + 64, gen_out);
-    logits_all_kernel<<<2048, 256, 0, stream>>>(item_emb, xl_all, out);
+    hipMemsetAsync(bar, 0, 114688, stream);
+
+    mega_kernel<<<GRID_, 256, 0, stream>>>(
+        ht, item_emb, pos_emb, ipw, ipb, ow, ob, l1w, l1b, l2w, l2b,
+        f1w, f1b, f2w, f2b, bar, cand, emb8, y_last, gen_idx,
+        y0, hbuf, hbuf2, xl_all, out, gen_out);
 }
```
